# Optimization experiments

Measured on AMD Instinct MI355X. Metric: run time of the kernel, lower is better.

The kernel has to match this reference:

```python
import jax, jax.numpy as jnp
import numpy as np
import math

MODEL_DIM = 1024
BATCH = 4
SEQ = 4096
ATTENTION_INPUT = 'both'


def make_F(model_dim, attention_input):
    F = jnp.zeros((model_dim, model_dim), dtype=jnp.float32)
    if attention_input == 'both':
        a = model_dim
    else:
        a = model_dim // 2
    # faithful to source: elif means 'both' only hits the first branch
    if attention_input in ['both', 'only_sem']:
        idx = jnp.arange(0, a)
        F = F.at[idx, idx].set(1.0)
    elif attention_input in ['only_pos']:
        idx = jnp.arange(a, 2 * a)
        F = F.at[idx, idx].set(1.0)
    return F


def setup_inputs() -> dict:
    key = jax.random.key(0)
    kx, kq, kk, kv = jax.random.split(key, 4)
    x = jax.random.normal(kx, (BATCH, SEQ, MODEL_DIM), dtype=jnp.float32)
    Q = jax.random.normal(kq, (MODEL_DIM, MODEL_DIM), dtype=jnp.float32) / math.sqrt(MODEL_DIM)
    K = jax.random.normal(kk, (MODEL_DIM, MODEL_DIM), dtype=jnp.float32) / math.sqrt(MODEL_DIM)
    V = jax.random.normal(kv, (MODEL_DIM, MODEL_DIM), dtype=jnp.float32) / math.sqrt(MODEL_DIM)
    return {"x": x, "Q": Q, "K": K, "V": V}


def reference(x, Q, K, V):
    model_dim = Q.shape[0]
    F = make_F(model_dim, ATTENTION_INPUT)
    Qx = x @ F @ Q            # [B, S, D]
    Kx = x @ F @ K            # [B, S, D]
    Vx = x @ V                # [B, S, D]
    scores = jnp.einsum('bqd,bkd->bqk', Qx, Kx) / math.sqrt(model_dim)  # [B, S, S]
    seq = x.shape[1]
    causal_mask = jnp.triu(jnp.ones((seq, seq), dtype=bool), k=1)       # True above diagonal
    scores = jnp.where(causal_mask, -jnp.inf, scores)
    probs = jax.nn.softmax(scores, axis=-1)
    return jnp.einsum('bqk,bkd->bqd', probs, Vx)
```

## Files before the change

### kernel.cpp

```cpp
#include <hip/hip_runtime.h>
#include <cstdint>
#include <cstddef>
#include <cmath>


typedef unsigned short u16;
typedef __bf16  bf16x8 __attribute__((ext_vector_type(8)));
typedef float   f32x4  __attribute__((ext_vector_type(4)));
typedef unsigned short u16x4 __attribute__((ext_vector_type(4)));

typedef __attribute__((address_space(1))) void gvoid;
typedef __attribute__((address_space(3))) void lvoid;

__device__ __forceinline__ u16 f2bf(float f) {
  union { float f; unsigned u; } v; v.f = f;
  unsigned u = v.u;
  u += 0x7FFFu + ((u >> 16) & 1u);
  return (u16)(u >> 16);
}
__device__ __forceinline__ float bf2f(u16 h) {
  union { unsigned u; float f; } v; v.u = ((unsigned)h) << 16;
  return v.f;
}
__device__ __forceinline__ void async16(const void* g, void* l) {
  __builtin_amdgcn_global_load_lds((gvoid*)(void*)g, (lvoid*)l, 16, 0, 0);
}

__global__ void __launch_bounds__(256) cvt_f32_bf16(const float4* __restrict__ in,
                                                    u16* __restrict__ out, int n4) {
  int i = blockIdx.x * 256 + threadIdx.x;
  if (i >= n4) return;
  float4 v = in[i];
  u16x4 o = { f2bf(v.x), f2bf(v.y), f2bf(v.z), f2bf(v.w) };
  *(u16x4*)(out + 4 * (size_t)i) = o;
}

__device__ __forceinline__ u16 to_bfs(float v, float s) { return f2bf(v * s); }
__device__ __forceinline__ u16 to_bfs(u16 v, float)     { return v; }

template <typename TIN>
__global__ void __launch_bounds__(256) transpose_to_bf16(
    const TIN* __restrict__ in, u16* __restrict__ out,
    int rows, int cols, long inStride, long outStride, float scale) {
  __shared__ u16 t[64][68];
  int rt = blockIdx.x * 64, ct = blockIdx.y * 64;
  long ib = (long)blockIdx.z * inStride, ob = (long)blockIdx.z * outStride;
  int tx = threadIdx.x & 63, ty = threadIdx.x >> 6;
#pragma unroll
  for (int r = ty; r < 64; r += 4)
    t[r][tx] = to_bfs(in[ib + (long)(rt + r) * cols + ct + tx], scale);
  __syncthreads();
#pragma unroll
  for (int r = ty; r < 64; r += 4)
    out[ob + (long)(ct + r) * rows + rt + tx] = t[tx][r];
}


#define G8_BAR()  __builtin_amdgcn_s_barrier()
#define G8_VMC4() asm volatile("s_waitcnt vmcnt(4)" ::: "memory")
#define G8_VMC0() asm volatile("s_waitcnt vmcnt(0)" ::: "memory")

#define G8_STAGE_A(bn, kp, kb) do { \
    async16(Ag + (kb) + a0, (void*)&As[bn][kp][l0]); \
    async16(Ag + (kb) + a1, (void*)&As[bn][kp][l1]); } while (0)
#define G8_STAGE_B(bn, kp, kb) do { \
    async16(Bg + (kb) + b0, (void*)&Bs[bn][kp][l0]); \
    async16(Bg + (kb) + b1, (void*)&Bs[bn][kp][l1]); } while (0)

#define G8_LDA(bc, kp, ch) do { _Pragma("unroll") \
    for (int u_ = 0; u_ < 4; ++u_) \
      af[u_] = *(const bf16x8*)&As[bc][kp][(wm * 128 + (ch) * 64 + u_ * 16 + lr) * 32 + swq]; \
  } while (0)
#define G8_LDB(bc, kp) do { _Pragma("unroll") \
    for (int j_ = 0; j_ < 4; ++j_) \
      bf[j_] = *(const bf16x8*)&Bs[bc][kp][(wn * 64 + j_ * 16 + lr) * 32 + swq]; \
  } while (0)

#define G8_MFMA(ch) do { \
    __builtin_amdgcn_s_setprio(1); \
    _Pragma("unroll") for (int u_ = 0; u_ < 4; ++u_) \
      _Pragma("unroll") for (int j_ = 0; j_ < 4; ++j_) \
        acc[(ch) * 4 + u_][j_] = __builtin_amdgcn_mfma_f32_16x16x32_bf16( \
            af[u_], bf[j_], acc[(ch) * 4 + u_][j_], 0, 0, 0); \
    __builtin_amdgcn_s_setprio(0); } while (0)

#define G8_TILE(bc, bn, kt, kn) do { \
    bf16x8 af[4], bf[4]; \
     \
    G8_LDB(bc, 0); G8_LDA(bc, 0, 0); \
    G8_STAGE_A(bn, 0, (kn)); \
    G8_BAR(); G8_MFMA(0); G8_BAR(); \
     \
    G8_LDA(bc, 0, 1); \
    G8_STAGE_B(bn, 0, (kn)); \
    G8_BAR(); G8_MFMA(1); G8_VMC4(); G8_BAR(); \
     \
    G8_LDB(bc, 1); G8_LDA(bc, 1, 0); \
    G8_STAGE_A(bn, 1, (kn) + 32); \
    G8_BAR(); G8_MFMA(0); G8_BAR(); \
     \
    G8_LDA(bc, 1, 1); \
    G8_STAGE_B(bn, 1, (kn) + 32); \
    G8_BAR(); G8_MFMA(1); G8_VMC4(); G8_BAR(); } while (0)

template <bool OUTF32, bool TRI>
__global__ void __launch_bounds__(512, 2) gemm8_bt(
    const u16* __restrict__ A, const u16* __restrict__ Bt, void* __restrict__ C,
    int K, int lda, int ldb, int ldc,
    long aStride, long bStride, long cStride, float alpha) {
  int mt, nt;
  if (TRI) {
    const int bid = blockIdx.x;
    int m = (int)((sqrtf(8.0f * (float)bid + 1.0f) - 1.0f) * 0.5f);
    while ((m + 1) * (m + 2) / 2 <= bid) ++m;
    while (m * (m + 1) / 2 > bid) --m;
    mt = m; nt = bid - m * (m + 1) / 2;
  } else { mt = blockIdx.x; nt = blockIdx.y; }
  const int bz = blockIdx.z;
  const int tid = threadIdx.x, wv = tid >> 6, ln = tid & 63;
  const int wm = wv & 1, wn = wv >> 1;
  const int lr = ln & 15, quad = ln >> 4;
  const int swq = (quad ^ ((lr >> 1) & 3)) << 3;
  const u16* Ag = A + (long)bz * aStride + (long)(mt * 256) * lda;
  const u16* Bg = Bt + (long)bz * bStride + (long)(nt * 256) * ldb;

  __shared__ __align__(16) __bf16 As[2][2][256 * 32];
  __shared__ __align__(16) __bf16 Bs[2][2][256 * 32];

  f32x4 acc[8][4];
#pragma unroll
  for (int i = 0; i < 8; ++i)
#pragma unroll
    for (int j = 0; j < 4; ++j)
#pragma unroll
      for (int r = 0; r < 4; ++r) acc[i][j][r] = 0.f;

  const int c0 = tid, c1 = tid + 512;
  const int r0 = c0 >> 2, r1 = c1 >> 2;
  const long a0 = (long)r0 * lda + (((c0 & 3) ^ ((r0 >> 1) & 3)) << 3);
  const long a1 = (long)r1 * lda + (((c1 & 3) ^ ((r1 >> 1) & 3)) << 3);
  const long b0 = (long)r0 * ldb + (((c0 & 3) ^ ((r0 >> 1) & 3)) << 3);
  const long b1 = (long)r1 * ldb + (((c1 & 3) ^ ((r1 >> 1) & 3)) << 3);
  const int l0 = c0 * 8, l1 = c1 * 8;

  const int kend = K;

  G8_STAGE_A(0, 0, 0); G8_STAGE_B(0, 0, 0);
  G8_STAGE_A(0, 1, 32); G8_STAGE_B(0, 1, 32);
  G8_VMC4(); G8_BAR();

  for (int k0 = 0; k0 < kend; k0 += 128) {
    const long kn0 = (k0 + 64  < kend) ? (long)k0 + 64  : (long)k0;
    const long kn1 = (k0 + 128 < kend) ? (long)k0 + 128 : (long)k0 + 64;
    G8_TILE(0, 1, k0, kn0);
    G8_TILE(1, 0, k0 + 64, kn1);
  }
  G8_VMC0();

  const long cb = (long)bz * cStride;
#pragma unroll
  for (int i = 0; i < 8; ++i) {
    int row0 = mt * 256 + wm * 128 + i * 16 + quad * 4;
#pragma unroll
    for (int j = 0; j < 4; ++j) {
      int col = nt * 256 + wn * 64 + j * 16 + lr;
#pragma unroll
      for (int r = 0; r < 4; ++r) {
        float v = acc[i][j][r] * alpha;
        long idx = cb + (long)(row0 + r) * ldc + col;
        if (OUTF32) ((float*)C)[idx] = v;
        else        ((u16*)C)[idx]  = f2bf(v);
      }
    }
  }
}

template <bool OUTF32, bool TRI, bool CK, int BM>
__global__ void __launch_bounds__(256, BM == 256 ? 2 : 4) gemm_bt(
    const u16* __restrict__ A, const u16* __restrict__ Bt, void* __restrict__ C,
    int K, int lda, int ldb, int ldc,
    long aStride, long bStride, long cStride, float alpha) {
  constexpr int MR = BM / 32;
  constexpr int AQ = BM / 64;
  int mt, nt, bz;
  if (TRI) {
    const int bid = blockIdx.x;
    int m = (int)((sqrtf(4.0f * (float)bid + 1.0f) - 1.0f) * 0.5f);
    while ((m + 1) * (m + 2) <= bid) ++m;
    while (m * (m + 1) > bid) --m;
    mt = m; nt = bid - m * (m + 1);
    bz = blockIdx.z;
  } else if (CK) {
    const int id = blockIdx.x;
    const int g = id & 7, mid = (id >> 3) & 31, hi = id >> 8;
    bz = mid & 3; nt = mid >> 2;
    mt = (hi == 0) ? 31 - g : (hi == 1) ? 16 + g : (hi == 2) ? 15 - g : g;
  } else {
    mt = blockIdx.x; nt = blockIdx.y; bz = blockIdx.z;
  }
  const int tid = threadIdx.x, wv = tid >> 6, ln = tid & 63;
  const u16* Ag = A + (long)bz * aStride + (long)(mt * BM) * lda;
  const u16* Bg = Bt + (long)bz * bStride + (long)(nt * 128) * ldb;

  __shared__ __align__(16) __bf16 As[2][BM * 32];
  __shared__ __align__(16) __bf16 Bs[2][128 * 32];

  f32x4 acc[MR][4];
#pragma unroll
  for (int i = 0; i < MR; ++i)
#pragma unroll
    for (int j = 0; j < 4; ++j)
#pragma unroll
      for (int r = 0; r < 4; ++r) acc[i][j][r] = 0.f;

  const int kend = CK ? (((mt + 1) * BM < K) ? (mt + 1) * BM : K) : K;
  const int wm = wv & 1, wn = wv >> 1;
  const int mrow = wm * (BM / 2), nrow = wn * 64;
  const int lr = ln & 15, quad = ln >> 4;

  long aOff[AQ]; int aLds[AQ];
#pragma unroll
  for (int q = 0; q < AQ; ++q) {
    int c = q * 256 + tid, row = c >> 2, c8i = c & 3;
    aOff[q] = (long)row * lda + ((c8i ^ ((row >> 1) & 3)) << 3);
    aLds[q] = c * 8;
  }
  long bOff[2]; int bLds[2];
#pragma unroll
  for (int q = 0; q < 2; ++q) {
    int c = q * 256 + tid, row = c >> 2, c8i = c & 3;
    bOff[q] = (long)row * ldb + ((c8i ^ ((row >> 1) & 3)) << 3);
    bLds[q] = c * 8;
  }
  const int swq = (quad ^ ((lr >> 1) & 3)) << 3;

  for (int k0 = 0; k0 < kend; k0 += 64) {
#pragma unroll
    for (int p = 0; p < 2; ++p) {
      const long kk = k0 + p * 32;
#pragma unroll
      for (int q = 0; q < AQ; ++q)
        async16(Ag + kk + aOff[q], (char*)As[p] + aLds[q] * 2);
#pragma unroll
      for (int q = 0; q < 2; ++q)
        async16(Bg + kk + bOff[q], (char*)Bs[p] + bLds[q] * 2);
    }
    __syncthreads();
#pragma unroll
    for (int p = 0; p < 2; ++p) {
      bf16x8 af[MR], bfr[4];
#pragma unroll
      for (int u = 0; u < MR; ++u)
        af[u] = *(const bf16x8*)&As[p][(mrow + u * 16 + lr) * 32 + swq];
#pragma unroll
      for (int j = 0; j < 4; ++j)
        bfr[j] = *(const bf16x8*)&Bs[p][(nrow + j * 16 + lr) * 32 + swq];
#pragma unroll
      for (int u = 0; u < MR; ++u)
#pragma unroll
        for (int j = 0; j < 4; ++j)
          acc[u][j] = __builtin_amdgcn_mfma_f32_16x16x32_bf16(af[u], bfr[j], acc[u][j], 0, 0, 0);
    }
    __syncthreads();
  }

  const long cb = (long)bz * cStride;
#pragma unroll
  for (int i = 0; i < MR; ++i) {
    int row0 = mt * BM + mrow + i * 16 + quad * 4;
#pragma unroll
    for (int j = 0; j < 4; ++j) {
      int col = nt * 128 + nrow + j * 16 + lr;
#pragma unroll
      for (int r = 0; r < 4; ++r) {
        float v = acc[i][j][r] * alpha;
        long idx = cb + (long)(row0 + r) * ldc + col;
        if (OUTF32) ((float*)C)[idx] = v;
        else        ((u16*)C)[idx]  = f2bf(v);
      }
    }
  }
}

__global__ void __launch_bounds__(256) softmax_rows(u16* __restrict__ Sb,
                                                    long bStride, int S) {
  const int row = blockIdx.x;
  u16* p = Sb + (long)blockIdx.y * bStride + (long)row * S;
  const int L = row + 1;
  const int Lpad = (L + 255) & ~255;
  const int tid = threadIdx.x, ln = tid & 63, wv = tid >> 6;
  __shared__ float red[8];

  float vals[16];
  float lmax = -3.4e38f;
#pragma unroll
  for (int k = 0; k < 16; ++k) {
    int j = tid + k * 256;
    if (j < L) { float v = bf2f(p[j]); vals[k] = v; lmax = fmaxf(lmax, v); }
  }
#pragma unroll
  for (int o = 32; o > 0; o >>= 1) lmax = fmaxf(lmax, __shfl_down(lmax, o));
  if (ln == 0) red[wv] = lmax;
  __syncthreads();
  float m = fmaxf(fmaxf(red[0], red[1]), fmaxf(red[2], red[3]));

  float lsum = 0.f;
#pragma unroll
  for (int k = 0; k < 16; ++k) {
    int j = tid + k * 256;
    if (j < L) { float e = __expf(vals[k] - m); vals[k] = e; lsum += e; }
  }
#pragma unroll
  for (int o = 32; o > 0; o >>= 1) lsum += __shfl_down(lsum, o);
  __syncthreads();
  if (ln == 0) red[wv] = lsum;
  __syncthreads();
  float inv = 1.f / (red[0] + red[1] + red[2] + red[3]);
#pragma unroll
  for (int k = 0; k < 16; ++k) {
    int j = tid + k * 256;
    if (j < L) p[j] = f2bf(vals[k] * inv);
  }
  for (int j = L + tid; j < Lpad; j += 256) p[j] = 0;
}

extern "C" void kernel_launch(void* const* d_in, const int* in_sizes, int n_in,
                              void* d_out, int out_size, void* d_ws, size_t ws_size,
                              hipStream_t stream) {
  const float* x = (const float*)d_in[0];
  const float* Q = (const float*)d_in[1];
  const float* K = (const float*)d_in[2];
  const float* V = (const float*)d_in[3];
  float* out = (float*)d_out;

  constexpr int  Bb = 4, S = 4096, D = 1024;
  constexpr long MB = 1024 * 1024;
  if (ws_size < (size_t)(224 * MB)) return;

  char* ws = (char*)d_ws;
  u16* QKx  = (u16*)(ws);
  u16* Vxt  = (u16*)(ws + 64 * MB);
  u16* Sb   = (u16*)(ws + 96 * MB);
  u16* Vtmp = (u16*)(ws + 96 * MB);
  u16* XB   = (u16*)(ws + 128 * MB);
  u16* WTqk = (u16*)(ws + 160 * MB);
  u16* WTv  = (u16*)(ws + 164 * MB);

  const long SD = (long)S * D, SS = (long)S * S;

  cvt_f32_bf16<<<dim3((Bb * S * D / 4) / 256), 256, 0, stream>>>(
      (const float4*)x, XB, Bb * S * D / 4);

  transpose_to_bf16<float><<<dim3(16, 16, 1), 256, 0, stream>>>(
      Q, WTqk, 1024, 1024, 0, 0, 0.03125f);
  transpose_to_bf16<float><<<dim3(16, 16, 1), 256, 0, stream>>>(
      K, WTqk + 1024 * 1024, 1024, 1024, 0, 0, 1.0f);
  transpose_to_bf16<float><<<dim3(16, 16, 1), 256, 0, stream>>>(
      V, WTv, 1024, 1024, 0, 0, 1.0f);

  gemm8_bt<false, false><<<dim3(64, 8, 1), 512, 0, stream>>>(
      XB, WTqk, QKx, 1024, 1024, 1024, 2048, 0, 0, 0, 1.0f);
  gemm8_bt<false, false><<<dim3(64, 4, 1), 512, 0, stream>>>(
      XB, WTv, Vtmp, 1024, 1024, 1024, 1024, 0, 0, 0, 1.0f);

  transpose_to_bf16<u16><<<dim3(64, 16, Bb), 256, 0, stream>>>(
      Vtmp, Vxt, S, D, SD, SD, 1.0f);

  gemm8_bt<false, true><<<dim3(136, 1, Bb), 512, 0, stream>>>(
      QKx, QKx + 1024, Sb, 1024, 2048, 2048, S, 2 * SD, 2 * SD, SS, 1.0f);

  softmax_rows<<<dim3(S, Bb), 256, 0, stream>>>(Sb, SS, S);

  gemm_bt<true, false, true, 128><<<dim3(1024, 1, 1), 256, 0, stream>>>(
      Sb, Vxt, out, S, S, S, D, SS, SD, SD, 1.0f);
}
```

Baseline: 505.6 us.

## Compute transposed V projection directly via swapped GEMM; vectorize softmax row access

The V projection is now computed as WTv times XB^T, writing Vx already transposed into one [D, B*S] buffer. This removes the separate GEMM-then-transpose pass and its intermediate buffer, and the final PV GEMM is re-strided to read the new layout. The softmax kernel now gives each thread 16 contiguous elements loaded and stored as 8-wide vectors, and writes the zero padding inside the same vector stores. Contiguous per-thread chunks give strided access across lanes, which may hurt coalescing compared with the old interleaved layout.

```diff
diff --git a/kernel.cpp b/kernel.cpp
--- a/kernel.cpp
+++ b/kernel.cpp
@@ -8,6 +8,7 @@
 typedef __bf16  bf16x8 __attribute__((ext_vector_type(8)));
 typedef float   f32x4  __attribute__((ext_vector_type(4)));
 typedef unsigned short u16x4 __attribute__((ext_vector_type(4)));
+typedef unsigned short u16x8 __attribute__((ext_vector_type(8)));
 
 typedef __attribute__((address_space(1))) void gvoid;
 typedef __attribute__((address_space(3))) void lvoid;
@@ -34,9 +35,6 @@
   u16x4 o = { f2bf(v.x), f2bf(v.y), f2bf(v.z), f2bf(v.w) };
   *(u16x4*)(out + 4 * (size_t)i) = o;
 }
-
-__device__ __forceinline__ u16 to_bfs(float v, float s) { return f2bf(v * s); }
-__device__ __forceinline__ u16 to_bfs(u16 v, float)     { return v; }
 
 template <typename TIN>
 __global__ void __launch_bounds__(256) transpose_to_bf16(
@@ -48,7 +46,7 @@
   int tx = threadIdx.x & 63, ty = threadIdx.x >> 6;
 #pragma unroll
   for (int r = ty; r < 64; r += 4)
-    t[r][tx] = to_bfs(in[ib + (long)(rt + r) * cols + ct + tx], scale);
+    t[r][tx] = f2bf((float)in[ib + (long)(rt + r) * cols + ct + tx] * scale);
   __syncthreads();
 #pragma unroll
   for (int r = ty; r < 64; r += 4)
@@ -289,14 +287,25 @@
   const int L = row + 1;
   const int Lpad = (L + 255) & ~255;
   const int tid = threadIdx.x, ln = tid & 63, wv = tid >> 6;
-  __shared__ float red[8];
+  const int base0 = tid * 16;
+  __shared__ float red[4];
 
   float vals[16];
   float lmax = -3.4e38f;
 #pragma unroll
-  for (int k = 0; k < 16; ++k) {
-    int j = tid + k * 256;
-    if (j < L) { float v = bf2f(p[j]); vals[k] = v; lmax = fmaxf(lmax, v); }
+  for (int k = 0; k < 2; ++k) {
+    const int b = base0 + k * 8;
+    if (b < L) {
+      u16x8 v = *(const u16x8*)(p + b);
+#pragma unroll
+      for (int e = 0; e < 8; ++e) {
+        if (b + e < L) { float f = bf2f(v[e]); vals[k * 8 + e] = f; lmax = fmaxf(lmax, f); }
+        else vals[k * 8 + e] = 0.f;
+      }
+    } else {
+#pragma unroll
+      for (int e = 0; e < 8; ++e) vals[k * 8 + e] = 0.f;
+    }
   }
 #pragma unroll
   for (int o = 32; o > 0; o >>= 1) lmax = fmaxf(lmax, __shfl_down(lmax, o));
@@ -306,9 +315,13 @@
 
   float lsum = 0.f;
 #pragma unroll
-  for (int k = 0; k < 16; ++k) {
-    int j = tid + k * 256;
-    if (j < L) { float e = __expf(vals[k] - m); vals[k] = e; lsum += e; }
+  for (int k = 0; k < 2; ++k) {
+    const int b = base0 + k * 8;
+#pragma unroll
+    for (int e = 0; e < 8; ++e) {
+      float ex = (b + e < L) ? __expf(vals[k * 8 + e] - m) : 0.f;
+      vals[k * 8 + e] = ex; lsum += ex;
+    }
   }
 #pragma unroll
   for (int o = 32; o > 0; o >>= 1) lsum += __shfl_down(lsum, o);
@@ -317,11 +330,15 @@
   __syncthreads();
   float inv = 1.f / (red[0] + red[1] + red[2] + red[3]);
 #pragma unroll
-  for (int k = 0; k < 16; ++k) {
-    int j = tid + k * 256;
-    if (j < L) p[j] = f2bf(vals[k] * inv);
-  }
-  for (int j = L + tid; j < Lpad; j += 256) p[j] = 0;
+  for (int k = 0; k < 2; ++k) {
+    const int b = base0 + k * 8;
+    if (b < Lpad) {
+      u16x8 o;
+#pragma unroll
+      for (int e = 0; e < 8; ++e) o[e] = f2bf(vals[k * 8 + e] * inv);
+      *(u16x8*)(p + b) = o;
+    }
+  }
 }
 
 extern "C" void kernel_launch(void* const* d_in, const int* in_sizes, int n_in,
@@ -341,7 +358,6 @@
   u16* QKx  = (u16*)(ws);
   u16* Vxt  = (u16*)(ws + 64 * MB);
   u16* Sb   = (u16*)(ws + 96 * MB);
-  u16* Vtmp = (u16*)(ws + 96 * MB);
   u16* XB   = (u16*)(ws + 128 * MB);
   u16* WTqk = (u16*)(ws + 160 * MB);
   u16* WTv  = (u16*)(ws + 164 * MB);
@@ -360,11 +376,8 @@
 
   gemm8_bt<false, false><<<dim3(64, 8, 1), 512, 0, stream>>>(
       XB, WTqk, QKx, 1024, 1024, 1024, 2048, 0, 0, 0, 1.0f);
-  gemm8_bt<false, false><<<dim3(64, 4, 1), 512, 0, stream>>>(
-      XB, WTv, Vtmp, 1024, 1024, 1024, 1024, 0, 0, 0, 1.0f);
-
-  transpose_to_bf16<u16><<<dim3(64, 16, Bb), 256, 0, stream>>>(
-      Vtmp, Vxt, S, D, SD, SD, 1.0f);
+  gemm8_bt<false, false><<<dim3(4, 64, 1), 512, 0, stream>>>(
+      WTv, XB, Vxt, 1024, 1024, 1024, 16384, 0, 0, 0, 1.0f);
 
   gemm8_bt<false, true><<<dim3(136, 1, Bb), 512, 0, stream>>>(
       QKx, QKx + 1024, Sb, 1024, 2048, 2048, S, 2 * SD, 2 * SD, SS, 1.0f);
@@ -372,5 +385,5 @@
   softmax_rows<<<dim3(S, Bb), 256, 0, stream>>>(Sb, SS, S);
 
   gemm_bt<true, false, true, 128><<<dim3(1024, 1, 1), 256, 0, stream>>>(
-      Sb, Vxt, out, S, S, S, D, SS, SD, SD, 1.0f);
-}
+      Sb, Vxt, out, S, S, 16384, D, SS, 4096, SD, 1.0f);
+}
```

New measurement: 475.4 us. 1.06x faster.
